# Kernel tuning notes

Hardware: AMD Instinct MI355X
Metric: run time of the kernel (lower is better)

## Reference

```python
import jax, jax.numpy as jnp
import numpy as np

B, T, N, D, FF = 4, 288, 207, 152, 256  # batch, time, nodes, model_dim, feed_forward_dim


def setup_inputs() -> dict:
    key = jax.random.key(0)
    k0, k1, k2 = jax.random.split(key, 3)
    X = jax.random.normal(k0, (B, T, N, D), dtype=jnp.float32)
    Wq = jax.random.normal(k1, (FF, N * D), dtype=jnp.float32) * 0.02
    bq = jnp.zeros((FF,), jnp.float32)
    Wk = jax.random.normal(k2, (FF, N * D), dtype=jnp.float32) * 0.02
    bk = jnp.zeros((FF,), jnp.float32)
    return {"X": X, "Wq": Wq, "bq": bq, "Wk": Wk, "bk": bk, "K": 6}


def reference(X, Wq, bq, Wk, bk, K):
    b, t, n, d = X.shape
    x_pack = X.reshape(b, t, n * d)                      # (B,T,N*D)
    q = x_pack @ Wq.T + bq                               # (B,T,FF)
    k = x_pack @ Wk.T + bk                               # (B,T,FF)
    q_fft = jnp.fft.rfft(q, axis=-1)                     # (B,T,FF//2+1) complex
    k_fft = jnp.fft.rfft(k, axis=-1)
    # cross-correlation in frequency domain: (B,T,T,F)
    cross_fft = q_fft[:, :, None, :] * jnp.conj(k_fft)[:, None, :, :]
    # NOTE: original uses ifft (not irfft) over the rfft-length axis, takes real part
    cross_corr = jnp.fft.ifft(cross_fft, axis=-1).real   # (B,T,T,F)
    corr_matrix = cross_corr.mean(axis=-1).mean(axis=0)  # (T,T)
    corr_matrix = jnp.where(jnp.eye(t, dtype=bool), -jnp.inf, corr_matrix)
    topk_values, topk_indices = jax.lax.top_k(corr_matrix, K)   # (T,K), descending values
    order = jnp.argsort(topk_indices, axis=-1)                  # ascending index order
    sorted_values = jnp.take_along_axis(topk_values, order, axis=-1)   # (T,K)
    sorted_indices = jnp.take_along_axis(topk_indices, order, axis=-1)  # (T,K)
    # gather X at selected timesteps: (B,T,K,N,D) == X[b, sorted_indices[t,k], n, d]
    sorted_values_from_X = X[:, sorted_indices]          # (B,T,K,N,D)
    return sorted_values, sorted_indices, sorted_values_from_X
```

## Files before the change

kernel.cpp:

```cpp
#include <hip/hip_runtime.h>
#include <math.h>

#define B_  4
#define T_  288
#define N_  207
#define D_  152
#define FF_ 256
#define ND_ (N_*D_)
#define ND4 (ND_/4)
#define K_  6

typedef float vfloat4 __attribute__((ext_vector_type(4)));

__global__ void colsum_kernel(const float* __restrict__ Wq,
                              const float* __restrict__ Wk,
                              float* __restrict__ wq_sum,
                              float* __restrict__ wk_sum) {
    int j = blockIdx.x * blockDim.x + threadIdx.x;
    if (j >= ND4) return;
    const vfloat4* W  = (const vfloat4*)((blockIdx.y == 0) ? Wq : Wk);
    vfloat4*      out = (vfloat4*)((blockIdx.y == 0) ? wq_sum : wk_sum);
    vfloat4 s = {0.f, 0.f, 0.f, 0.f};
    #pragma unroll 4
    for (int ff = 0; ff < FF_; ++ff)
        s += __builtin_nontemporal_load(&W[(size_t)ff * ND4 + j]);
    out[j] = s;
}

__global__ void biassum_kernel(const float* __restrict__ bq,
                               const float* __restrict__ bk,
                               float* __restrict__ bsum) {
    __shared__ float shq[256], shk[256];
    int tid = threadIdx.x;
    shq[tid] = bq[tid];
    shk[tid] = bk[tid];
    __syncthreads();
    for (int s = 128; s > 0; s >>= 1) {
        if (tid < s) { shq[tid] += shq[tid + s]; shk[tid] += shk[tid + s]; }
        __syncthreads();
    }
    if (tid == 0) { bsum[0] = shq[0]; bsum[1] = shk[0]; }
}

__global__ void rowdot_kernel(const float* __restrict__ X,
                              const float* __restrict__ wq_sum,
                              const float* __restrict__ wk_sum,
                              const float* __restrict__ bsum,
                              float* __restrict__ sq,
                              float* __restrict__ sk) {
    int row = blockIdx.x;
    int tid = threadIdx.x;
    const vfloat4* x4 = (const vfloat4*)(X + (size_t)row * ND_);
    const vfloat4* q4 = (const vfloat4*)wq_sum;
    const vfloat4* k4 = (const vfloat4*)wk_sum;
    float pq = 0.f, pk = 0.f;
    for (int j = tid; j < ND4; j += 256) {
        vfloat4 xv = x4[j];
        vfloat4 qv = q4[j];
        vfloat4 kv = k4[j];
        pq += xv.x*qv.x + xv.y*qv.y + xv.z*qv.z + xv.w*qv.w;
        pk += xv.x*kv.x + xv.y*kv.y + xv.z*kv.z + xv.w*kv.w;
    }
    __shared__ float shq[256], shk[256];
    shq[tid] = pq; shk[tid] = pk;
    __syncthreads();
    for (int s = 128; s > 0; s >>= 1) {
        if (tid < s) { shq[tid] += shq[tid + s]; shk[tid] += shk[tid + s]; }
        __syncthreads();
    }
    if (tid == 0) {
        sq[row] = shq[0] + bsum[0];
        sk[row] = shk[0] + bsum[1];
    }
}

#define SLOTS 5
__global__ __launch_bounds__(64) void topk_kernel(
                            const float* __restrict__ sq,
                            const float* __restrict__ sk,
                            float* __restrict__ out_vals,
                            float* __restrict__ out_idx_f,
                            int*   __restrict__ out_idx_i) {
    int t1   = blockIdx.x;
    int lane = threadIdx.x;
    float sq0 = sq[0*T_ + t1], sq1 = sq[1*T_ + t1];
    float sq2 = sq[2*T_ + t1], sq3 = sq[3*T_ + t1];

    float v[SLOTS]; int vi[SLOTS];
    #pragma unroll
    for (int s = 0; s < SLOTS; ++s) {
        int t2 = lane + s * 64;
        if (t2 < T_ && t2 != t1) {
            float c = sq0*sk[0*T_ + t2] + sq1*sk[1*T_ + t2]
                    + sq2*sk[2*T_ + t2] + sq3*sk[3*T_ + t2];
            v[s]  = c * (1.0f / (129.0f * (float)B_));
            vi[s] = t2;
        } else {
            v[s]  = -INFINITY;
            vi[s] = 0x7fffffff;
        }
    }

    float tv[K_]; int ti[K_];
    for (int k = 0; k < K_; ++k) {
        float bv = v[0]; int bi = vi[0];
        #pragma unroll
        for (int s = 1; s < SLOTS; ++s) {
            if (v[s] > bv || (v[s] == bv && vi[s] < bi)) { bv = v[s]; bi = vi[s]; }
        }
        #pragma unroll
        for (int off = 32; off > 0; off >>= 1) {
            float ov = __shfl_xor(bv, off);
            int   oi = __shfl_xor(bi, off);
            if (ov > bv || (ov == bv && oi < bi)) { bv = ov; bi = oi; }
        }
        tv[k] = bv; ti[k] = bi;
        #pragma unroll
        for (int s = 0; s < SLOTS; ++s)
            if (vi[s] == bi) { v[s] = -INFINITY; vi[s] = 0x7fffffff; }
    }

    if (lane == 0) {
        for (int a = 1; a < K_; ++a) {
            float vv = tv[a]; int ii = ti[a]; int b = a - 1;
            while (b >= 0 && ti[b] > ii) { tv[b+1] = tv[b]; ti[b+1] = ti[b]; --b; }
            tv[b+1] = vv; ti[b+1] = ii;
        }
        for (int k = 0; k < K_; ++k) {
            out_vals [t1*K_ + k] = tv[k];
            out_idx_f[t1*K_ + k] = (float)ti[k];
            out_idx_i[t1*K_ + k] = ti[k];
        }
    }
}

__global__ void gather_kernel(const float* __restrict__ X,
                              const int* __restrict__ idx,
                              float* __restrict__ out3) {
    int bid = blockIdx.x;
    int b   = bid / (T_ * K_);
    int rk  = bid % (T_ * K_);
    int src_t = idx[rk];
    const vfloat4* src = (const vfloat4*)(X + ((size_t)b * T_ + src_t) * ND_);
    vfloat4*       dst = (vfloat4*)(out3 + (size_t)bid * ND_);
    for (int j = threadIdx.x; j < ND4; j += 256) {
        vfloat4 val = src[j];
        __builtin_nontemporal_store(val, &dst[j]);
    }
}

extern "C" void kernel_launch(void* const* d_in, const int* in_sizes, int n_in,
                              void* d_out, int out_size, void* d_ws, size_t ws_size,
                              hipStream_t stream) {
    const float* X  = (const float*)d_in[0];
    const float* Wq = (const float*)d_in[1];
    const float* bq = (const float*)d_in[2];
    const float* Wk = (const float*)d_in[3];
    const float* bk = (const float*)d_in[4];

    float* ws = (float*)d_ws;
    float* wq_sum = ws;
    float* wk_sum = ws + ND_;
    float* bsum   = ws + 2*ND_;
    float* sq     = ws + 2*ND_ + 4;
    float* sk     = sq + B_*T_;
    int*   idx_i  = (int*)(sk + B_*T_);

    float* out_vals  = (float*)d_out;
    float* out_idx_f = out_vals + T_*K_;
    float* out3      = out_idx_f + T_*K_;

    dim3 g1((ND4 + 255)/256, 2);
    colsum_kernel<<<g1, 256, 0, stream>>>(Wq, Wk, wq_sum, wk_sum);
    biassum_kernel<<<1, 256, 0, stream>>>(bq, bk, bsum);
    rowdot_kernel<<<B_*T_, 256, 0, stream>>>(X, wq_sum, wk_sum, bsum, sq, sk);
    topk_kernel<<<T_, 64, 0, stream>>>(sq, sk, out_vals, out_idx_f, idx_i);
    gather_kernel<<<B_*T_*K_, 256, 0, stream>>>(X, idx_i, out3);
}
```

Baseline: 289.0 us.

## Invert gather to per-source scatter so each X row is read once

Top-k now builds inverse lists: for each source timestep, an atomic counter and a list of destination (t,k) slots, with the counters zeroed inside rowdot. The gather kernel is reorganised as a grid over chunk, source timestep and batch. Each block loads a chunk of the source row into registers once and writes it to every destination that selected it, so X reads no longer repeat per duplicate selection. The trade-offs are atomics in top-k and uneven per-block work, since popular sources write many times. Writes, which dominate, are unchanged.

```diff
diff --git a/kernel.cpp b/kernel.cpp
--- a/kernel.cpp
+++ b/kernel.cpp
@@ -9,6 +9,8 @@
 #define ND_ (N_*D_)
 #define ND4 (ND_/4)
 #define K_  6
+#define CH_ 8
+#define CHSZ 984
 
 typedef float vfloat4 __attribute__((ext_vector_type(4)));
 
@@ -47,9 +49,11 @@
                               const float* __restrict__ wk_sum,
                               const float* __restrict__ bsum,
                               float* __restrict__ sq,
-                              float* __restrict__ sk) {
+                              float* __restrict__ sk,
+                              int*   __restrict__ cnt) {
     int row = blockIdx.x;
     int tid = threadIdx.x;
+    if (row < T_ && tid == 0) cnt[row] = 0;
     const vfloat4* x4 = (const vfloat4*)(X + (size_t)row * ND_);
     const vfloat4* q4 = (const vfloat4*)wq_sum;
     const vfloat4* k4 = (const vfloat4*)wk_sum;
@@ -80,7 +84,8 @@
                             const float* __restrict__ sk,
                             float* __restrict__ out_vals,
                             float* __restrict__ out_idx_f,
-                            int*   __restrict__ out_idx_i) {
+                            int*   __restrict__ cnt,
+                            int*   __restrict__ lists) {
     int t1   = blockIdx.x;
     int lane = threadIdx.x;
     float sq0 = sq[0*T_ + t1], sq1 = sq[1*T_ + t1];
@@ -129,23 +134,42 @@
         for (int k = 0; k < K_; ++k) {
             out_vals [t1*K_ + k] = tv[k];
             out_idx_f[t1*K_ + k] = (float)ti[k];
-            out_idx_i[t1*K_ + k] = ti[k];
-        }
-    }
-}
-
-__global__ void gather_kernel(const float* __restrict__ X,
-                              const int* __restrict__ idx,
+            int src = ti[k];
+            int pos = atomicAdd(&cnt[src], 1);
+            lists[src * T_ + pos] = t1 * K_ + k;
+        }
+    }
+}
+
+__global__ __launch_bounds__(256) void gather_kernel(
+                              const float* __restrict__ X,
+                              const int* __restrict__ cnt,
+                              const int* __restrict__ lists,
                               float* __restrict__ out3) {
-    int bid = blockIdx.x;
-    int b   = bid / (T_ * K_);
-    int rk  = bid % (T_ * K_);
-    int src_t = idx[rk];
-    const vfloat4* src = (const vfloat4*)(X + ((size_t)b * T_ + src_t) * ND_);
-    vfloat4*       dst = (vfloat4*)(out3 + (size_t)bid * ND_);
-    for (int j = threadIdx.x; j < ND4; j += 256) {
-        vfloat4 val = src[j];
-        __builtin_nontemporal_store(val, &dst[j]);
+    int c   = blockIdx.x;
+    int src = blockIdx.y;
+    int b   = blockIdx.z;
+    int n = cnt[src];
+    if (n == 0) return;
+    const int j0 = c * CHSZ;
+    const int j1 = (j0 + CHSZ < ND4) ? (j0 + CHSZ) : ND4;
+    const vfloat4* srcp = (const vfloat4*)(X + ((size_t)b * T_ + src) * ND_);
+    const int* lst = lists + src * T_;
+
+    vfloat4 r[4];
+    #pragma unroll
+    for (int u = 0; u < 4; ++u) {
+        int j = j0 + (int)threadIdx.x + u * 256;
+        if (j < j1) r[u] = srcp[j];
+    }
+    for (int e = 0; e < n; ++e) {
+        int rk = lst[e];
+        vfloat4* dst = (vfloat4*)(out3 + ((size_t)b * (T_ * K_) + rk) * ND_);
+        #pragma unroll
+        for (int u = 0; u < 4; ++u) {
+            int j = j0 + (int)threadIdx.x + u * 256;
+            if (j < j1) __builtin_nontemporal_store(r[u], &dst[j]);
+        }
     }
 }
 
@@ -164,7 +188,8 @@
     float* bsum   = ws + 2*ND_;
     float* sq     = ws + 2*ND_ + 4;
     float* sk     = sq + B_*T_;
-    int*   idx_i  = (int*)(sk + B_*T_);
+    int*   cnt    = (int*)(sk + B_*T_);
+    int*   lists  = cnt + T_;
 
     float* out_vals  = (float*)d_out;
     float* out_idx_f = out_vals + T_*K_;
@@ -173,7 +198,7 @@
     dim3 g1((ND4 + 255)/256, 2);
     colsum_kernel<<<g1, 256, 0, stream>>>(Wq, Wk, wq_sum, wk_sum);
     biassum_kernel<<<1, 256, 0, stream>>>(bq, bk, bsum);
-    rowdot_kernel<<<B_*T_, 256, 0, stream>>>(X, wq_sum, wk_sum, bsum, sq, sk);
-    topk_kernel<<<T_, 64, 0, stream>>>(sq, sk, out_vals, out_idx_f, idx_i);
-    gather_kernel<<<B_*T_*K_, 256, 0, stream>>>(X, idx_i, out3);
-}
+    rowdot_kernel<<<B_*T_, 256, 0, stream>>>(X, wq_sum, wk_sum, bsum, sq, sk, cnt);
+    topk_kernel<<<T_, 64, 0, stream>>>(sq, sk, out_vals, out_idx_f, cnt, lists);
+    gather_kernel<<<dim3(CH_, T_, B_), 256, 0, stream>>>(X, cnt, lists, out3);
+}
```

Result: slower. 304.9 us (+5.5%).
